# Kernel tuning notes

Measured on AMD Instinct MI355X. Metric: run time of the kernel, lower is better.

Reference implementation:

```python
import jax, jax.numpy as jnp
import numpy as np

DIMS = [1024, 2048, 1024, 1024]


def setup_inputs() -> dict:
    key = jax.random.key(0)
    ks = jax.random.split(key, 13)
    d_in, h1, h2, d_out = DIMS
    s = lambda k, shape, fan_in: jax.random.normal(k, shape, dtype=jnp.float32) / np.sqrt(fan_in)
    return {
        "x": jax.random.normal(ks[0], (4, 2048, d_in), dtype=jnp.float32),
        "w1": s(ks[1], (h1, d_in), d_in), "b1": jnp.zeros((h1,), jnp.float32),
        "w2": s(ks[2], (h2, h1), h1), "b2": jnp.zeros((h2,), jnp.float32),
        "wq": s(ks[3], (h2, h2), h2), "bq": jnp.zeros((h2,), jnp.float32),
        "wk": s(ks[4], (h2, h2), h2), "bk": jnp.zeros((h2,), jnp.float32),
        "wv": s(ks[5], (h2, h2), h2), "bv": jnp.zeros((h2,), jnp.float32),
        "wo": s(ks[6], (d_out, h2), h2), "bo": jnp.zeros((d_out,), jnp.float32),
    }


def reference(x, w1, b1, w2, b2, wq, bq, wk, bk, wv, bv, wo, bo):
    # MLP: Linear + ReLU twice (torch Linear: x @ W^T + b)
    h = jax.nn.relu(jnp.einsum('bsd,hd->bsh', x, w1) + b1)
    h = jax.nn.relu(jnp.einsum('bsh,eh->bse', h, w2) + b2)
    # Self-attention (single head over full hidden_dim)
    q = jnp.einsum('bse,fe->bsf', h, wq) + bq
    k = jnp.einsum('bse,fe->bsf', h, wk) + bk
    v = jnp.einsum('bse,fe->bsf', h, wv) + bv
    hidden_dim = wq.shape[0]
    scores = jnp.einsum('bsf,btf->bst', q, k) / jnp.sqrt(jnp.float32(hidden_dim))
    attn = jax.nn.softmax(scores, axis=-1)
    ctx = jnp.einsum('bst,btf->bsf', attn, v) + v  # residual with V
    return jnp.einsum('bsf,of->bso', ctx, wo) + bo
```

## Files before the change

kernel.cpp:

```cpp
#include <hip/hip_runtime.h>
#include <hip/hip_bf16.h>

typedef __bf16 bf16;
typedef bf16 bf16x8 __attribute__((ext_vector_type(8)));
typedef float f32x4 __attribute__((ext_vector_type(4)));

#define EPI_BIAS_RELU  0
#define EPI_BIAS_BF16  1
#define EPI_PLAIN_BF16 2
#define EPI_RESID      3
#define EPI_BIAS_F32   4

__device__ __forceinline__ void lds_load16(const bf16* g, bf16* l) {
  __builtin_amdgcn_global_load_lds((__attribute__((address_space(1))) void*)g,
                                   (__attribute__((address_space(3))) void*)l,
                                   16, 0, 0);
}

template<int N> __device__ __forceinline__ void vmw() {
  if constexpr (N == 0) asm volatile("s_waitcnt vmcnt(0)" ::: "memory");
  else if constexpr (N == 4) asm volatile("s_waitcnt vmcnt(4)" ::: "memory");
  else if constexpr (N == 6) asm volatile("s_waitcnt vmcnt(6)" ::: "memory");
}
__device__ __forceinline__ void barrier() { asm volatile("s_barrier" ::: "memory"); }

template<int EPI, int BM>
__global__ __launch_bounds__(512, 2)
void gemm8p(const bf16* __restrict__ A, const bf16* __restrict__ B,
            void* __restrict__ Cv, const float* __restrict__ bias,
            const bf16* __restrict__ resid,
            int K, int lda, int ldb, int ldc,
            long long sAz, long long sBz, long long sCz, long long sRz)
{
  constexpr int BN = 256, BK = 64;
  constexpr int WM = BM / 2, WN = 64;
  constexpr int M_REP = WM / 16, N_REP = 4;
  constexpr int MH = M_REP / 2, NH = 2;
  constexpr int LA = BM / 128, LB = 2;
  constexpr int N3 = LA + LB + LA;

  __shared__ __align__(16) bf16 lA[2][BM * BK];
  __shared__ __align__(16) bf16 lB[2][BN * BK];

  const int gx = gridDim.x, gy = gridDim.y;
  const int nwg = gx * gy * gridDim.z;
  int o = (blockIdx.z * gy + blockIdx.y) * gx + blockIdx.x;
  o = (o & 7) * (nwg >> 3) + (o >> 3);
  const int bx = o % gx;
  const int rem = o / gx;
  const int by = rem % gy;
  const int z = rem / gy;

  const bf16* Ab = A + (size_t)z * sAz;
  const bf16* Bb = B + (size_t)z * sBz;
  const int row0 = by * BM, col0 = bx * BN;
  const int tid = threadIdx.x, w = tid >> 6, l = tid & 63;
  const int wr = w >> 2, wc = w & 3;

  const int srow = l >> 3, scb = (l & 7) ^ srow;
  const bf16* gA = Ab + (size_t)(row0 + w * 8 + srow) * lda + scb * 8;
  const bf16* gB = Bb + (size_t)(col0 + w * 8 + srow) * ldb + scb * 8;

  auto issueA = [&](int buf, int k0, int h) {
#pragma unroll
    for (int i = 0; i < LA; i++)
      lds_load16(gA + (size_t)(h * (BM / 2) + i * 64) * lda + k0,
                 &lA[buf][(h * (BM / 2) + i * 64 + w * 8) * BK]);
  };
  auto issueB = [&](int buf, int k0, int h) {
#pragma unroll
    for (int i = 0; i < LB; i++)
      lds_load16(gB + (size_t)(h * 128 + i * 64) * ldb + k0,
                 &lB[buf][(h * 128 + i * 64 + w * 8) * BK]);
  };

  const int fr = l & 15, fq = l >> 4, sw = fr & 7;

  bf16x8 aA0[MH][2], aA1[MH][2], bB0[NH][2], bB1[NH][2];
  f32x4 acc[M_REP][N_REP] = {};

  auto readA = [&](bf16x8 (&dst)[MH][2], int buf, int h) {
#pragma unroll
    for (int mm = 0; mm < MH; mm++) {
      const int r = h * (BM / 2) + wr * (WM / 2) + mm * 16 + fr;
      const bf16* base = &lA[buf][r * BK];
#pragma unroll
      for (int kk = 0; kk < 2; kk++)
        dst[mm][kk] = *(const bf16x8*)(base + ((kk * 4 + fq) ^ sw) * 8);
    }
  };
  auto readB = [&](bf16x8 (&dst)[NH][2], int buf, int h) {
#pragma unroll
    for (int nn = 0; nn < NH; nn++) {
      const int r = h * 128 + wc * 32 + nn * 16 + fr;
      const bf16* base = &lB[buf][r * BK];
#pragma unroll
      for (int kk = 0; kk < 2; kk++)
        dst[nn][kk] = *(const bf16x8*)(base + ((kk * 4 + fq) ^ sw) * 8);
    }
  };
  auto quad = [&](const bf16x8 (&a)[MH][2], const bf16x8 (&b)[NH][2],
                  int mBase, int nBase) {
    __builtin_amdgcn_s_setprio(1);
#pragma unroll
    for (int mh = 0; mh < MH; mh++)
#pragma unroll
      for (int nh = 0; nh < NH; nh++)
#pragma unroll
        for (int kk = 0; kk < 2; kk++)
          acc[mBase + mh][nBase + nh] = __builtin_amdgcn_mfma_f32_16x16x32_bf16(
              a[mh][kk], b[nh][kk], acc[mBase + mh][nBase + nh], 0, 0, 0);
    __builtin_amdgcn_s_setprio(0);
  };

  const int NT = K / BK;
  issueA(0, 0, 0); issueB(0, 0, 0); issueA(0, 0, 1); issueB(0, 0, 1);
  issueA(1, BK, 0); issueB(1, BK, 0); issueA(1, BK, 1);
  vmw<N3>();
  barrier();

  for (int t = 0; t < NT; t++) {
    const int cur = t & 1, nxt = cur ^ 1;
    const bool s1 = (t + 1 < NT), s2 = (t + 2 < NT);
    const int k1 = (t + 1) * BK, k2 = (t + 2) * BK;
    readA(aA0, cur, 0);
    readB(bB0, cur, 0);
    if (s1) issueB(nxt, k1, 1);
    barrier();
    quad(aA0, bB0, 0, 0);
    barrier();
    readA(aA1, cur, 1);
    if (s2) issueA(cur, k2, 0);
    barrier();
    quad(aA1, bB0, MH, 0);
    barrier();
    readB(bB1, cur, 1);
    if (s2) issueB(cur, k2, 0);
    barrier();
    quad(aA1, bB1, MH, NH);
    barrier();
    if (s2) { issueA(cur, k2, 1); vmw<N3>(); }
    else vmw<0>();
    barrier();
    quad(aA0, bB1, 0, NH);
    barrier();
  }

#pragma unroll
  for (int m = 0; m < M_REP; m++) {
#pragma unroll
    for (int n = 0; n < N_REP; n++) {
      const int col = col0 + (n / NH) * 128 + wc * 32 + (n % NH) * 16 + fr;
#pragma unroll
      for (int j = 0; j < 4; j++) {
        const int rrow = row0 + (m / MH) * (BM / 2) + wr * (WM / 2) + (m % MH) * 16 + fq * 4 + j;
        const float val = acc[m][n][j];
        if constexpr (EPI == EPI_PLAIN_BF16) {
          bf16* Cp = (bf16*)Cv + (size_t)z * sCz;
          Cp[(size_t)rrow * ldc + col] = (bf16)val;
        } else if constexpr (EPI == EPI_BIAS_F32) {
          float* Cp = (float*)Cv;
          Cp[(size_t)rrow * ldc + col] = val + bias[col];
        } else if constexpr (EPI == EPI_BIAS_BF16) {
          bf16* Cp = (bf16*)Cv;
          Cp[(size_t)rrow * ldc + col] = (bf16)(val + bias[col]);
        } else if constexpr (EPI == EPI_BIAS_RELU) {
          bf16* Cp = (bf16*)Cv;
          Cp[(size_t)rrow * ldc + col] = (bf16)fmaxf(val + bias[col], 0.f);
        } else {
          bf16* Cp = (bf16*)Cv + (size_t)z * sCz;
          const bf16* Rp = resid + (size_t)z * sRz;
          Cp[(size_t)rrow * ldc + col] = (bf16)(val + (float)Rp[(size_t)rrow * ldc + col]);
        }
      }
    }
  }
}

__global__ __launch_bounds__(256)
void cast_f32_to_bf16(const float* __restrict__ in, bf16* __restrict__ out,
                      int n8, float scale) {
  int i = blockIdx.x * 256 + threadIdx.x;
  if (i >= n8) return;
  const float4* p = (const float4*)in;
  float4 a = p[2 * i], b = p[2 * i + 1];
  bf16x8 o;
  o[0] = (bf16)(a.x * scale); o[1] = (bf16)(a.y * scale);
  o[2] = (bf16)(a.z * scale); o[3] = (bf16)(a.w * scale);
  o[4] = (bf16)(b.x * scale); o[5] = (bf16)(b.y * scale);
  o[6] = (bf16)(b.z * scale); o[7] = (bf16)(b.w * scale);
  ((bf16x8*)out)[i] = o;
}

__global__ __launch_bounds__(256)
void pack_bias_qk(const float* __restrict__ bq, const float* __restrict__ bk,
                  float* __restrict__ o) {
  int i = blockIdx.x * 256 + threadIdx.x;
  o[i] = (i < 1024) ? bq[i] * 0.03125f : bk[i - 1024];
}

__global__ __launch_bounds__(256)
void transpose_bf16(const bf16* __restrict__ in, bf16* __restrict__ out, int R, int C) {
  __shared__ bf16 t[64][72];
  const bf16* ib = in + (size_t)blockIdx.z * R * C;
  bf16* ob = out + (size_t)blockIdx.z * R * C;
  const int r0 = blockIdx.y * 64, c0 = blockIdx.x * 64;
  const int tid = threadIdx.x;
#pragma unroll
  for (int p = 0; p < 2; p++) {
    int r = p * 32 + tid / 8, cc = (tid % 8) * 8;
    bf16x8 vv = *(const bf16x8*)(ib + (size_t)(r0 + r) * C + c0 + cc);
#pragma unroll
    for (int j = 0; j < 8; j++) t[r][cc + j] = vv[j];
  }
  __syncthreads();
#pragma unroll
  for (int p = 0; p < 2; p++) {
    int r = p * 32 + tid / 8, cc = (tid % 8) * 8;
    bf16x8 o;
#pragma unroll
    for (int j = 0; j < 8; j++) o[j] = t[cc + j][r];
    *(bf16x8*)(ob + (size_t)(c0 + r) * R + r0 + cc) = o;
  }
}

__global__ __launch_bounds__(256)
void softmax_rows(const bf16* __restrict__ S, bf16* __restrict__ P) {
  const size_t row = blockIdx.x;
  const int t = threadIdx.x, wv = t >> 6, ln = t & 63;
  bf16x8 v8 = ((const bf16x8*)(S + row * 2048))[t];
  float v[8];
#pragma unroll
  for (int j = 0; j < 8; j++) v[j] = (float)v8[j];
  float m = v[0];
#pragma unroll
  for (int j = 1; j < 8; j++) m = fmaxf(m, v[j]);
  for (int o = 32; o; o >>= 1) m = fmaxf(m, __shfl_xor(m, o));
  __shared__ float redm[4], reds[4];
  if (ln == 0) redm[wv] = m;
  __syncthreads();
  m = fmaxf(fmaxf(redm[0], redm[1]), fmaxf(redm[2], redm[3]));
  float e[8], s = 0.f;
#pragma unroll
  for (int j = 0; j < 8; j++) { e[j] = __expf(v[j] - m); s += e[j]; }
  for (int o = 32; o; o >>= 1) s += __shfl_xor(s, o);
  if (ln == 0) reds[wv] = s;
  __syncthreads();
  s = reds[0] + reds[1] + reds[2] + reds[3];
  const float inv = 1.f / s;
  bf16x8 o8;
#pragma unroll
  for (int j = 0; j < 8; j++) o8[j] = (bf16)(e[j] * inv);
  ((bf16x8*)(P + row * 2048))[t] = o8;
}

extern "C" void kernel_launch(void* const* d_in, const int* in_sizes, int n_in,
                              void* d_out, int out_size, void* d_ws, size_t ws_size,
                              hipStream_t stream) {
  const float* x  = (const float*)d_in[0];
  const float* w1 = (const float*)d_in[1];
  const float* b1 = (const float*)d_in[2];
  const float* w2 = (const float*)d_in[3];
  const float* b2 = (const float*)d_in[4];
  const float* wq = (const float*)d_in[5];
  const float* bq = (const float*)d_in[6];
  const float* wk = (const float*)d_in[7];
  const float* bk = (const float*)d_in[8];
  const float* wv = (const float*)d_in[9];
  const float* bv = (const float*)d_in[10];
  const float* wo = (const float*)d_in[11];
  const float* bo = (const float*)d_in[12];
  float* out = (float*)d_out;

  char* ws = (char*)d_ws;
  const size_t MB = 1024ull * 1024ull;
  if (ws_size < 144 * MB) return;

  bf16* w1b  = (bf16*)(ws + 0 * MB);
  bf16* w2b  = (bf16*)(ws + 4 * MB);
  bf16* wqkb = (bf16*)(ws + 8 * MB);
  bf16* wvb  = (bf16*)(ws + 12 * MB);
  bf16* wob  = (bf16*)(ws + 14 * MB);
  float* bqk = (float*)(ws + 16 * MB);
  bf16* xb  = (bf16*)(ws + 17 * MB);
  bf16* h1  = (bf16*)(ws + 33 * MB);
  bf16* h   = (bf16*)(ws + 65 * MB);
  bf16* qk  = (bf16*)(ws + 81 * MB);
  bf16* vb  = (bf16*)(ws + 113 * MB);
  bf16* vT  = (bf16*)(ws + 17 * MB);
  bf16* S   = (bf16*)(ws + 33 * MB);
  bf16* P   = (bf16*)(ws + 65 * MB);
  bf16* ctx = (bf16*)(ws + 33 * MB);

  cast_f32_to_bf16<<<4096, 256, 0, stream>>>(x,  xb,  8192 * 1024 / 8, 1.f);
  cast_f32_to_bf16<<<1024, 256, 0, stream>>>(w1, w1b, 2048 * 1024 / 8, 1.f);
  cast_f32_to_bf16<<<1024, 256, 0, stream>>>(w2, w2b, 1024 * 2048 / 8, 1.f);
  cast_f32_to_bf16<<<512, 256, 0, stream>>>(wq, wqkb,                 1024 * 1024 / 8, 0.03125f);
  cast_f32_to_bf16<<<512, 256, 0, stream>>>(wk, wqkb + 1024 * 1024,   1024 * 1024 / 8, 1.f);
  cast_f32_to_bf16<<<512, 256, 0, stream>>>(wv, wvb, 1024 * 1024 / 8, 1.f);
  cast_f32_to_bf16<<<512, 256, 0, stream>>>(wo, wob, 1024 * 1024 / 8, 1.f);
  pack_bias_qk<<<8, 256, 0, stream>>>(bq, bk, bqk);

  gemm8p<EPI_BIAS_RELU, 256><<<dim3(8, 32, 1), 512, 0, stream>>>(
      xb, w1b, h1, b1, nullptr, 1024, 1024, 1024, 2048, 0, 0, 0, 0);
  gemm8p<EPI_BIAS_RELU, 128><<<dim3(4, 64, 1), 512, 0, stream>>>(
      h1, w2b, h, b2, nullptr, 2048, 2048, 2048, 1024, 0, 0, 0, 0);
  gemm8p<EPI_BIAS_BF16, 256><<<dim3(8, 32, 1), 512, 0, stream>>>(
      h, wqkb, qk, bqk, nullptr, 1024, 1024, 1024, 2048, 0, 0, 0, 0);
  gemm8p<EPI_BIAS_BF16, 128><<<dim3(4, 64, 1), 512, 0, stream>>>(
      h, wvb, vb, bv, nullptr, 1024, 1024, 1024, 1024, 0, 0, 0, 0);
  transpose_bf16<<<dim3(16, 32, 4), 256, 0, stream>>>(vb, vT, 2048, 1024);
  gemm8p<EPI_PLAIN_BF16, 256><<<dim3(8, 8, 4), 512, 0, stream>>>(
      qk, qk + 1024, S, nullptr, nullptr, 1024, 2048, 2048, 2048,
      2048LL * 2048, 2048LL * 2048, 2048LL * 2048, 0);
  softmax_rows<<<8192, 256, 0, stream>>>(S, P);
  gemm8p<EPI_RESID, 128><<<dim3(4, 16, 4), 512, 0, stream>>>(
      P, vT, ctx, nullptr, vb, 2048, 2048, 2048, 1024,
      2048LL * 2048, 1024LL * 2048, 2048LL * 1024, 2048LL * 1024);
  gemm8p<EPI_BIAS_F32, 128><<<dim3(4, 64, 1), 512, 0, stream>>>(
      ctx, wob, out, bo, nullptr, 1024, 1024, 1024, 1024, 0, 0, 0, 0);
}
```

Baseline: 286.2 us.

## Fuse QKV projection, merge casts, add 2-phase BM128 GEMM, in-place softmax

The Q, K and V projections now run as one GEMM with N=3072, with V read directly from the strided qkv buffer for the transpose and the residual. The seven cast launches become a single cast_all kernel, and softmax now writes in place. The templated GEMM is split into a BM=256 four-phase kernel and a new BM=128 two-phase kernel that loads the whole A tile once per K step and reuses it across both B halves. The aim is fewer launches, one fewer pass over h, and less LDS read traffic for the narrow GEMMs, at the cost of a different pipeline schedule and strided V accesses.

New measurement: 275.2 us. -3.8%, faster.

```diff
diff --git a/kernel.cpp b/kernel.cpp
--- a/kernel.cpp
+++ b/kernel.cpp
@@ -19,41 +19,36 @@
 
 template<int N> __device__ __forceinline__ void vmw() {
   if constexpr (N == 0) asm volatile("s_waitcnt vmcnt(0)" ::: "memory");
+  else if constexpr (N == 2) asm volatile("s_waitcnt vmcnt(2)" ::: "memory");
   else if constexpr (N == 4) asm volatile("s_waitcnt vmcnt(4)" ::: "memory");
   else if constexpr (N == 6) asm volatile("s_waitcnt vmcnt(6)" ::: "memory");
 }
 __device__ __forceinline__ void barrier() { asm volatile("s_barrier" ::: "memory"); }
 
-template<int EPI, int BM>
+template<int EPI>
 __global__ __launch_bounds__(512, 2)
-void gemm8p(const bf16* __restrict__ A, const bf16* __restrict__ B,
+void gemm4p(const bf16* __restrict__ A, const bf16* __restrict__ B,
             void* __restrict__ Cv, const float* __restrict__ bias,
             const bf16* __restrict__ resid,
-            int K, int lda, int ldb, int ldc,
+            int K, int lda, int ldb, int ldc, int ldr,
             long long sAz, long long sBz, long long sCz, long long sRz)
 {
-  constexpr int BN = 256, BK = 64;
-  constexpr int WM = BM / 2, WN = 64;
-  constexpr int M_REP = WM / 16, N_REP = 4;
-  constexpr int MH = M_REP / 2, NH = 2;
-  constexpr int LA = BM / 128, LB = 2;
-  constexpr int N3 = LA + LB + LA;
+  constexpr int BM = 256, BK = 64;
+  constexpr int M_REP = 8, N_REP = 4, MH = 4, NH = 2;
+  constexpr int LA = 2, LB = 2, N3 = LA + LB + LA;
 
   __shared__ __align__(16) bf16 lA[2][BM * BK];
-  __shared__ __align__(16) bf16 lB[2][BN * BK];
+  __shared__ __align__(16) bf16 lB[2][256 * BK];
 
   const int gx = gridDim.x, gy = gridDim.y;
   const int nwg = gx * gy * gridDim.z;
   int o = (blockIdx.z * gy + blockIdx.y) * gx + blockIdx.x;
   o = (o & 7) * (nwg >> 3) + (o >> 3);
-  const int bx = o % gx;
-  const int rem = o / gx;
-  const int by = rem % gy;
-  const int z = rem / gy;
+  const int bx = o % gx, rem = o / gx, by = rem % gy, z = rem / gy;
 
   const bf16* Ab = A + (size_t)z * sAz;
   const bf16* Bb = B + (size_t)z * sBz;
-  const int row0 = by * BM, col0 = bx * BN;
+  const int row0 = by * BM, col0 = bx * 256;
   const int tid = threadIdx.x, w = tid >> 6, l = tid & 63;
   const int wr = w >> 2, wc = w & 3;
 
@@ -64,8 +59,8 @@
   auto issueA = [&](int buf, int k0, int h) {
 #pragma unroll
     for (int i = 0; i < LA; i++)
-      lds_load16(gA + (size_t)(h * (BM / 2) + i * 64) * lda + k0,
-                 &lA[buf][(h * (BM / 2) + i * 64 + w * 8) * BK]);
+      lds_load16(gA + (size_t)(h * 128 + i * 64) * lda + k0,
+                 &lA[buf][(h * 128 + i * 64 + w * 8) * BK]);
   };
   auto issueB = [&](int buf, int k0, int h) {
 #pragma unroll
@@ -75,15 +70,13 @@
   };
 
   const int fr = l & 15, fq = l >> 4, sw = fr & 7;
-
   bf16x8 aA0[MH][2], aA1[MH][2], bB0[NH][2], bB1[NH][2];
   f32x4 acc[M_REP][N_REP] = {};
 
   auto readA = [&](bf16x8 (&dst)[MH][2], int buf, int h) {
 #pragma unroll
     for (int mm = 0; mm < MH; mm++) {
-      const int r = h * (BM / 2) + wr * (WM / 2) + mm * 16 + fr;
-      const bf16* base = &lA[buf][r * BK];
+      const bf16* base = &lA[buf][(h * 128 + wr * 64 + mm * 16 + fr) * BK];
 #pragma unroll
       for (int kk = 0; kk < 2; kk++)
         dst[mm][kk] = *(const bf16x8*)(base + ((kk * 4 + fq) ^ sw) * 8);
@@ -92,8 +85,7 @@
   auto readB = [&](bf16x8 (&dst)[NH][2], int buf, int h) {
 #pragma unroll
     for (int nn = 0; nn < NH; nn++) {
-      const int r = h * 128 + wc * 32 + nn * 16 + fr;
-      const bf16* base = &lB[buf][r * BK];
+      const bf16* base = &lB[buf][(h * 128 + wc * 32 + nn * 16 + fr) * BK];
 #pragma unroll
       for (int kk = 0; kk < 2; kk++)
         dst[nn][kk] = *(const bf16x8*)(base + ((kk * 4 + fq) ^ sw) * 8);
@@ -153,7 +145,7 @@
       const int col = col0 + (n / NH) * 128 + wc * 32 + (n % NH) * 16 + fr;
 #pragma unroll
       for (int j = 0; j < 4; j++) {
-        const int rrow = row0 + (m / MH) * (BM / 2) + wr * (WM / 2) + (m % MH) * 16 + fq * 4 + j;
+        const int rrow = row0 + (m / MH) * 128 + wr * 64 + (m % MH) * 16 + fq * 4 + j;
         const float val = acc[m][n][j];
         if constexpr (EPI == EPI_PLAIN_BF16) {
           bf16* Cp = (bf16*)Cv + (size_t)z * sCz;
@@ -170,46 +162,192 @@
         } else {
           bf16* Cp = (bf16*)Cv + (size_t)z * sCz;
           const bf16* Rp = resid + (size_t)z * sRz;
-          Cp[(size_t)rrow * ldc + col] = (bf16)(val + (float)Rp[(size_t)rrow * ldc + col]);
+          Cp[(size_t)rrow * ldc + col] = (bf16)(val + (float)Rp[(size_t)rrow * ldr + col]);
         }
       }
     }
   }
 }
 
+template<int EPI>
+__global__ __launch_bounds__(512, 2)
+void gemm2p(const bf16* __restrict__ A, const bf16* __restrict__ B,
+            void* __restrict__ Cv, const float* __restrict__ bias,
+            const bf16* __restrict__ resid,
+            int K, int lda, int ldb, int ldc, int ldr,
+            long long sAz, long long sBz, long long sCz, long long sRz)
+{
+  constexpr int BM = 128, BK = 64;
+  constexpr int M_REP = 4, NH = 2;
+
+  __shared__ __align__(16) bf16 lA[2][BM * BK];
+  __shared__ __align__(16) bf16 lB[2][256 * BK];
+
+  const int gx = gridDim.x, gy = gridDim.y;
+  const int nwg = gx * gy * gridDim.z;
+  int o = (blockIdx.z * gy + blockIdx.y) * gx + blockIdx.x;
+  o = (o & 7) * (nwg >> 3) + (o >> 3);
+  const int bx = o % gx, rem = o / gx, by = rem % gy, z = rem / gy;
+
+  const bf16* Ab = A + (size_t)z * sAz;
+  const bf16* Bb = B + (size_t)z * sBz;
+  const int row0 = by * BM, col0 = bx * 256;
+  const int tid = threadIdx.x, w = tid >> 6, l = tid & 63;
+  const int wr = w >> 2, wc = w & 3;
+
+  const int srow = l >> 3, scb = (l & 7) ^ srow;
+  const bf16* gA = Ab + (size_t)(row0 + w * 8 + srow) * lda + scb * 8;
+  const bf16* gB = Bb + (size_t)(col0 + w * 8 + srow) * ldb + scb * 8;
+
+  auto issueAfull = [&](int buf, int k0) {
+#pragma unroll
+    for (int i = 0; i < 2; i++)
+      lds_load16(gA + (size_t)(i * 64) * lda + k0,
+                 &lA[buf][(i * 64 + w * 8) * BK]);
+  };
+  auto issueBfull = [&](int buf, int k0) {
+#pragma unroll
+    for (int i = 0; i < 4; i++)
+      lds_load16(gB + (size_t)(i * 64) * ldb + k0,
+                 &lB[buf][(i * 64 + w * 8) * BK]);
+  };
+
+  const int fr = l & 15, fq = l >> 4, sw = fr & 7;
+  bf16x8 aA[M_REP][2], bB0[NH][2], bB1[NH][2];
+  f32x4 acc[M_REP][4] = {};
+
+  auto readAfull = [&](int buf) {
+#pragma unroll
+    for (int m = 0; m < M_REP; m++) {
+      const bf16* base = &lA[buf][(wr * 64 + m * 16 + fr) * BK];
+#pragma unroll
+      for (int kk = 0; kk < 2; kk++)
+        aA[m][kk] = *(const bf16x8*)(base + ((kk * 4 + fq) ^ sw) * 8);
+    }
+  };
+  auto readB = [&](bf16x8 (&dst)[NH][2], int buf, int h) {
+#pragma unroll
+    for (int nn = 0; nn < NH; nn++) {
+      const bf16* base = &lB[buf][(h * 128 + wc * 32 + nn * 16 + fr) * BK];
+#pragma unroll
+      for (int kk = 0; kk < 2; kk++)
+        dst[nn][kk] = *(const bf16x8*)(base + ((kk * 4 + fq) ^ sw) * 8);
+    }
+  };
+  auto quad2 = [&](const bf16x8 (&b)[NH][2], int nBase) {
+    __builtin_amdgcn_s_setprio(1);
+#pragma unroll
+    for (int m = 0; m < M_REP; m++)
+#pragma unroll
+      for (int nh = 0; nh < NH; nh++)
+#pragma unroll
+        for (int kk = 0; kk < 2; kk++)
+          acc[m][nBase + nh] = __builtin_amdgcn_mfma_f32_16x16x32_bf16(
+              aA[m][kk], b[nh][kk], acc[m][nBase + nh], 0, 0, 0);
+    __builtin_amdgcn_s_setprio(0);
+  };
+
+  const int NT = K / BK;
+  issueAfull(0, 0); issueBfull(0, 0); issueAfull(1, BK);
+  vmw<2>();
+  barrier();
+
+  for (int t = 0; t < NT; t++) {
+    const int cur = t & 1, nxt = cur ^ 1;
+    const bool s1 = (t + 1 < NT), s2 = (t + 2 < NT);
+    readAfull(cur);
+    readB(bB0, cur, 0);
+    if (s1) issueBfull(nxt, (t + 1) * BK);
+    barrier();
+    quad2(bB0, 0);
+    barrier();
+    readB(bB1, cur, 1);
+    if (s2) { issueAfull(cur, (t + 2) * BK); vmw<2>(); }
+    else vmw<0>();
+    barrier();
+    quad2(bB1, NH);
+    barrier();
+  }
+
+#pragma unroll
+  for (int m = 0; m < M_REP; m++) {
+#pragma unroll
+    for (int n = 0; n < 4; n++) {
+      const int col = col0 + (n / NH) * 128 + wc * 32 + (n % NH) * 16 + fr;
+#pragma unroll
+      for (int j = 0; j < 4; j++) {
+        const int rrow = row0 + wr * 64 + m * 16 + fq * 4 + j;
+        const float val = acc[m][n][j];
+        if constexpr (EPI == EPI_PLAIN_BF16) {
+          bf16* Cp = (bf16*)Cv + (size_t)z * sCz;
+          Cp[(size_t)rrow * ldc + col] = (bf16)val;
+        } else if constexpr (EPI == EPI_BIAS_F32) {
+          float* Cp = (float*)Cv;
+          Cp[(size_t)rrow * ldc + col] = val + bias[col];
+        } else if constexpr (EPI == EPI_BIAS_BF16) {
+          bf16* Cp = (bf16*)Cv;
+          Cp[(size_t)rrow * ldc + col] = (bf16)(val + bias[col]);
+        } else if constexpr (EPI == EPI_BIAS_RELU) {
+          bf16* Cp = (bf16*)Cv;
+          Cp[(size_t)rrow * ldc + col] = (bf16)fmaxf(val + bias[col], 0.f);
+        } else {
+          bf16* Cp = (bf16*)Cv + (size_t)z * sCz;
+          const bf16* Rp = resid + (size_t)z * sRz;
+          Cp[(size_t)rrow * ldc + col] = (bf16)(val + (float)Rp[(size_t)rrow * ldr + col]);
+        }
+      }
+    }
+  }
+}
+
 __global__ __launch_bounds__(256)
-void cast_f32_to_bf16(const float* __restrict__ in, bf16* __restrict__ out,
-                      int n8, float scale) {
+void cast_all(const float* __restrict__ x,  const float* __restrict__ w1,
+              const float* __restrict__ w2, const float* __restrict__ wq,
+              const float* __restrict__ wk, const float* __restrict__ wv,
+              const float* __restrict__ wo,
+              bf16* __restrict__ xb, bf16* __restrict__ w1b,
+              bf16* __restrict__ w2b, bf16* __restrict__ wqkvb,
+              bf16* __restrict__ wob) {
+  const int b = blockIdx.x;
+  const float* src; bf16* dst; int base; float scale = 1.f;
+  if (b < 4096)      { src = x;  dst = xb;    base = b; }
+  else if (b < 5120) { src = w1; dst = w1b;   base = b - 4096; }
+  else if (b < 6144) { src = w2; dst = w2b;   base = b - 5120; }
+  else if (b < 6656) { src = wq; dst = wqkvb;                base = b - 6144; scale = 0.03125f; }
+  else if (b < 7168) { src = wk; dst = wqkvb + (1 << 20);    base = b - 6656; }
+  else if (b < 7680) { src = wv; dst = wqkvb + (2 << 20);    base = b - 7168; }
+  else               { src = wo; dst = wob;   base = b - 7680; }
+  const int i = base * 256 + threadIdx.x;
+  const float4* p = (const float4*)src;
+  float4 a = p[2 * i], c = p[2 * i + 1];
+  bf16x8 o8;
+  o8[0] = (bf16)(a.x * scale); o8[1] = (bf16)(a.y * scale);
+  o8[2] = (bf16)(a.z * scale); o8[3] = (bf16)(a.w * scale);
+  o8[4] = (bf16)(c.x * scale); o8[5] = (bf16)(c.y * scale);
+  o8[6] = (bf16)(c.z * scale); o8[7] = (bf16)(c.w * scale);
+  ((bf16x8*)dst)[i] = o8;
+}
+
+__global__ __launch_bounds__(256)
+void pack_bias_qkv(const float* __restrict__ bq, const float* __restrict__ bk,
+                   const float* __restrict__ bv, float* __restrict__ o) {
   int i = blockIdx.x * 256 + threadIdx.x;
-  if (i >= n8) return;
-  const float4* p = (const float4*)in;
-  float4 a = p[2 * i], b = p[2 * i + 1];
-  bf16x8 o;
-  o[0] = (bf16)(a.x * scale); o[1] = (bf16)(a.y * scale);
-  o[2] = (bf16)(a.z * scale); o[3] = (bf16)(a.w * scale);
-  o[4] = (bf16)(b.x * scale); o[5] = (bf16)(b.y * scale);
-  o[6] = (bf16)(b.z * scale); o[7] = (bf16)(b.w * scale);
-  ((bf16x8*)out)[i] = o;
+  o[i] = (i < 1024) ? bq[i] * 0.03125f : (i < 2048 ? bk[i - 1024] : bv[i - 2048]);
 }
 
 __global__ __launch_bounds__(256)
-void pack_bias_qk(const float* __restrict__ bq, const float* __restrict__ bk,
-                  float* __restrict__ o) {
-  int i = blockIdx.x * 256 + threadIdx.x;
-  o[i] = (i < 1024) ? bq[i] * 0.03125f : bk[i - 1024];
-}
-
-__global__ __launch_bounds__(256)
-void transpose_bf16(const bf16* __restrict__ in, bf16* __restrict__ out, int R, int C) {
+void transpose_bf16(const bf16* __restrict__ in, bf16* __restrict__ out,
+                    int R, int C, int ldi,
+                    long long inZ, long long outZ) {
   __shared__ bf16 t[64][72];
-  const bf16* ib = in + (size_t)blockIdx.z * R * C;
-  bf16* ob = out + (size_t)blockIdx.z * R * C;
+  const bf16* ib = in + (size_t)blockIdx.z * inZ;
+  bf16* ob = out + (size_t)blockIdx.z * outZ;
   const int r0 = blockIdx.y * 64, c0 = blockIdx.x * 64;
   const int tid = threadIdx.x;
 #pragma unroll
   for (int p = 0; p < 2; p++) {
     int r = p * 32 + tid / 8, cc = (tid % 8) * 8;
-    bf16x8 vv = *(const bf16x8*)(ib + (size_t)(r0 + r) * C + c0 + cc);
+    bf16x8 vv = *(const bf16x8*)(ib + (size_t)(r0 + r) * ldi + c0 + cc);
 #pragma unroll
     for (int j = 0; j < 8; j++) t[r][cc + j] = vv[j];
   }
@@ -225,9 +363,9 @@
 }
 
 __global__ __launch_bounds__(256)
-void softmax_rows(const bf16* __restrict__ S, bf16* __restrict__ P) {
+void softmax_rows(bf16* __restrict__ S) {
   const size_t row = blockIdx.x;
-  const int t = threadIdx.x, wv = t >> 6, ln = t & 63;
+  const int t = threadIdx.x, wv_ = t >> 6, ln = t & 63;
   bf16x8 v8 = ((const bf16x8*)(S + row * 2048))[t];
   float v[8];
 #pragma unroll
@@ -237,21 +375,21 @@
   for (int j = 1; j < 8; j++) m = fmaxf(m, v[j]);
   for (int o = 32; o; o >>= 1) m = fmaxf(m, __shfl_xor(m, o));
   __shared__ float redm[4], reds[4];
-  if (ln == 0) redm[wv] = m;
+  if (ln == 0) redm[wv_] = m;
   __syncthreads();
   m = fmaxf(fmaxf(redm[0], redm[1]), fmaxf(redm[2], redm[3]));
   float e[8], s = 0.f;
 #pragma unroll
   for (int j = 0; j < 8; j++) { e[j] = __expf(v[j] - m); s += e[j]; }
   for (int o = 32; o; o >>= 1) s += __shfl_xor(s, o);
-  if (ln == 0) reds[wv] = s;
+  if (ln == 0) reds[wv_] = s;
   __syncthreads();
   s = reds[0] + reds[1] + reds[2] + reds[3];
   const float inv = 1.f / s;
   bf16x8 o8;
 #pragma unroll
   for (int j = 0; j < 8; j++) o8[j] = (bf16)(e[j] * inv);
-  ((bf16x8*)(P + row * 2048))[t] = o8;
+  ((bf16x8*)(S + row * 2048))[t] = o8;
 }
 
 extern "C" void kernel_launch(void* const* d_in, const int* in_sizes, int n_in,
@@ -274,49 +412,40 @@
 
   char* ws = (char*)d_ws;
   const size_t MB = 1024ull * 1024ull;
-  if (ws_size < 144 * MB) return;
-
-  bf16* w1b  = (bf16*)(ws + 0 * MB);
-  bf16* w2b  = (bf16*)(ws + 4 * MB);
-  bf16* wqkb = (bf16*)(ws + 8 * MB);
-  bf16* wvb  = (bf16*)(ws + 12 * MB);
-  bf16* wob  = (bf16*)(ws + 14 * MB);
-  float* bqk = (float*)(ws + 16 * MB);
+  if (ws_size < 130 * MB) return;
+
+  bf16* w1b   = (bf16*)(ws + 0 * MB);
+  bf16* w2b   = (bf16*)(ws + 4 * MB);
+  bf16* wqkvb = (bf16*)(ws + 8 * MB);
+  bf16* wob   = (bf16*)(ws + 14 * MB);
+  float* bqkv = (float*)(ws + 16 * MB);
   bf16* xb  = (bf16*)(ws + 17 * MB);
   bf16* h1  = (bf16*)(ws + 33 * MB);
   bf16* h   = (bf16*)(ws + 65 * MB);
-  bf16* qk  = (bf16*)(ws + 81 * MB);
-  bf16* vb  = (bf16*)(ws + 113 * MB);
+  bf16* qkv = (bf16*)(ws + 81 * MB);
   bf16* vT  = (bf16*)(ws + 17 * MB);
   bf16* S   = (bf16*)(ws + 33 * MB);
-  bf16* P   = (bf16*)(ws + 65 * MB);
-  bf16* ctx = (bf16*)(ws + 33 * MB);
-
-  cast_f32_to_bf16<<<4096, 256, 0, stream>>>(x,  xb,  8192 * 1024 / 8, 1.f);
-  cast_f32_to_bf16<<<1024, 256, 0, stream>>>(w1, w1b, 2048 * 1024 / 8, 1.f);
-  cast_f32_to_bf16<<<1024, 256, 0, stream>>>(w2, w2b, 1024 * 2048 / 8, 1.f);
-  cast_f32_to_bf16<<<512, 256, 0, stream>>>(wq, wqkb,                 1024 * 1024 / 8, 0.03125f);
-  cast_f32_to_bf16<<<512, 256, 0, stream>>>(wk, wqkb + 1024 * 1024,   1024 * 1024 / 8, 1.f);
-  cast_f32_to_bf16<<<512, 256, 0, stream>>>(wv, wvb, 1024 * 1024 / 8, 1.f);
-  cast_f32_to_bf16<<<512, 256, 0, stream>>>(wo, wob, 1024 * 1024 / 8, 1.f);
-  pack_bias_qk<<<8, 256, 0, stream>>>(bq, bk, bqk);
-
-  gemm8p<EPI_BIAS_RELU, 256><<<dim3(8, 32, 1), 512, 0, stream>>>(
-      xb, w1b, h1, b1, nullptr, 1024, 1024, 1024, 2048, 0, 0, 0, 0);
-  gemm8p<EPI_BIAS_RELU, 128><<<dim3(4, 64, 1), 512, 0, stream>>>(
-      h1, w2b, h, b2, nullptr, 2048, 2048, 2048, 1024, 0, 0, 0, 0);
-  gemm8p<EPI_BIAS_BF16, 256><<<dim3(8, 32, 1), 512, 0, stream>>>(
-      h, wqkb, qk, bqk, nullptr, 1024, 1024, 1024, 2048, 0, 0, 0, 0);
-  gemm8p<EPI_BIAS_BF16, 128><<<dim3(4, 64, 1), 512, 0, stream>>>(
-      h, wvb, vb, bv, nullptr, 1024, 1024, 1024, 1024, 0, 0, 0, 0);
-  transpose_bf16<<<dim3(16, 32, 4), 256, 0, stream>>>(vb, vT, 2048, 1024);
-  gemm8p<EPI_PLAIN_BF16, 256><<<dim3(8, 8, 4), 512, 0, stream>>>(
-      qk, qk + 1024, S, nullptr, nullptr, 1024, 2048, 2048, 2048,
-      2048LL * 2048, 2048LL * 2048, 2048LL * 2048, 0);
-  softmax_rows<<<8192, 256, 0, stream>>>(S, P);
-  gemm8p<EPI_RESID, 128><<<dim3(4, 16, 4), 512, 0, stream>>>(
-      P, vT, ctx, nullptr, vb, 2048, 2048, 2048, 1024,
-      2048LL * 2048, 1024LL * 2048, 2048LL * 1024, 2048LL * 1024);
-  gemm8p<EPI_BIAS_F32, 128><<<dim3(4, 64, 1), 512, 0, stream>>>(
-      ctx, wob, out, bo, nullptr, 1024, 1024, 1024, 1024, 0, 0, 0, 0);
-}
+  bf16* ctx = (bf16*)(ws + 65 * MB);
+
+  cast_all<<<8192, 256, 0, stream>>>(x, w1, w2, wq, wk, wv, wo,
+                                     xb, w1b, w2b, wqkvb, wob);
+  pack_bias_qkv<<<12, 256, 0, stream>>>(bq, bk, bv, bqkv);
+
+  gemm4p<EPI_BIAS_RELU><<<dim3(8, 32, 1), 512, 0, stream>>>(
+      xb, w1b, h1, b1, nullptr, 1024, 1024, 1024, 2048, 0, 0, 0, 0, 0);
+  gemm2p<EPI_BIAS_RELU><<<dim3(4, 64, 1), 512, 0, stream>>>(
+      h1, w2b, h, b2, nullptr, 2048, 2048, 2048, 1024, 0, 0, 0, 0, 0);
+  gemm4p<EPI_BIAS_BF16><<<dim3(12, 32, 1), 512, 0, stream>>>(
+      h, wqkvb, qkv, bqkv, nullptr, 1024, 1024, 1024, 3072, 0, 0, 0, 0, 0);
+  transpose_bf16<<<dim3(16, 32, 4), 256, 0, stream>>>(
+      qkv + 2048, vT, 2048, 1024, 3072, 2048LL * 3072, 1024LL * 2048);
+  gemm4p<EPI_PLAIN_BF16><<<dim3(8, 8, 4), 512, 0, stream>>>(
+      qkv, qkv + 1024, S, nullptr, nullptr, 1024, 3072, 3072, 2048, 0,
+      2048LL * 3072, 2048LL * 3072, 2048LL * 2048, 0);
+  softmax_rows<<<8192, 256, 0, stream>>>(S);
+  gemm2p<EPI_RESID><<<dim3(4, 16, 4), 512, 0, stream>>>(
+      S, vT, ctx, nullptr, qkv + 2048, 2048, 2048, 2048, 1024, 3072,
+      2048LL * 2048, 1024LL * 2048, 2048LL * 1024, 2048LL * 3072);
+  gemm2p<EPI_BIAS_F32><<<dim3(4, 64, 1), 512, 0, stream>>>(
+      ctx, wob, out, bo, nullptr, 1024, 1024, 1024, 1024, 0, 0, 0, 0, 0);
+}
```
